# Optimization experiments

Measured on AMD Instinct MI355X. Metric: run time of the kernel, lower is better.

Reference implementation:

```python
import jax, jax.numpy as jnp
import numpy as np

N = 50000
IN_CH = 128
OUT_CH = 64
H1, C1 = 8, 8


def gat_layer(x, src, dst, W, att_src, att_dst, bias, heads, out_ch, concat, n_nodes):
    # x: [N, F_in]; W: [F_in, heads*out_ch]; att_*: [heads, out_ch]; bias: [heads*out_ch] or [out_ch]
    h = (x @ W).reshape(n_nodes, heads, out_ch)              # [N,H,C]
    a_src = jnp.einsum('nhc,hc->nh', h, att_src)             # [N,H]
    a_dst = jnp.einsum('nhc,hc->nh', h, att_dst)             # [N,H]
    e = jax.nn.leaky_relu(a_src[src] + a_dst[dst], 0.2)      # [E,H]
    # segment softmax over incoming edges of each dst node
    m = jax.ops.segment_max(e, dst, num_segments=n_nodes)    # [N,H]
    p = jnp.exp(e - m[dst])                                  # [E,H]
    s = jax.ops.segment_sum(p, dst, num_segments=n_nodes)    # [N,H]
    alpha = p / (s[dst] + 1e-16)                             # [E,H]
    out = jax.ops.segment_sum(h[src] * alpha[:, :, None], dst, num_segments=n_nodes)  # [N,H,C]
    out = out.reshape(n_nodes, heads * out_ch) if concat else out.mean(axis=1)
    return out + bias


def setup_inputs() -> dict:
    key = jax.random.key(0)
    ks = jax.random.split(key, 12)
    E = 1600000
    x = jax.random.normal(ks[0], (N, IN_CH), dtype=jnp.float32)
    edge_index = jax.random.randint(ks[1], (2, E), 0, N, dtype=jnp.int64)
    sc = 0.1
    return {
        'x': x,
        'edge_index': edge_index,
        'W1': jax.random.normal(ks[2], (IN_CH, H1 * C1), dtype=jnp.float32) * sc,
        'att_src1': jax.random.normal(ks[3], (H1, C1), dtype=jnp.float32) * sc,
        'att_dst1': jax.random.normal(ks[4], (H1, C1), dtype=jnp.float32) * sc,
        'b1': jnp.zeros((H1 * C1,), dtype=jnp.float32),
        'W2': jax.random.normal(ks[5], (H1 * C1, OUT_CH), dtype=jnp.float32) * sc,
        'att_src2': jax.random.normal(ks[6], (1, OUT_CH), dtype=jnp.float32) * sc,
        'att_dst2': jax.random.normal(ks[7], (1, OUT_CH), dtype=jnp.float32) * sc,
        'b2': jnp.zeros((OUT_CH,), dtype=jnp.float32),
        'lin_W': jax.random.normal(ks[8], (OUT_CH, 1), dtype=jnp.float32) * sc,
        'lin_b': jnp.zeros((1,), dtype=jnp.float32),
    }


def reference(x, edge_index, W1, att_src1, att_dst1, b1, W2, att_src2, att_dst2, b2, lin_W, lin_b):
    # add self loops (PyG GATConv default)
    loops = jnp.arange(N, dtype=edge_index.dtype)
    src = jnp.concatenate([edge_index[0], loops])
    dst = jnp.concatenate([edge_index[1], loops])
    # dropout layers are identity in eval mode
    h = gat_layer(x, src, dst, W1, att_src1, att_dst1, b1, H1, C1, True, N)
    h = jax.nn.elu(h)
    h = gat_layer(h, src, dst, W2, att_src2, att_dst2, b2, 1, OUT_CH, False, N)
    return h @ lin_W + lin_b
```

## Files before the change

### kernel.cpp

```cpp
#include <hip/hip_runtime.h>
#include <hip/hip_bf16.h>
#include <math.h>

#define NN     50000
#define FIN    128
#define F1     64
#define NH1    8
#define F2     64

#define BSH    256
#define NB     ((NN + BSH - 1) / BSH)
#define BCAP   9472
#define PREB   13
#define MG1B   ((NN + 255) / 256)

typedef __bf16 bf16x8 __attribute__((ext_vector_type(8)));
typedef float  f32x4  __attribute__((ext_vector_type(4)));
typedef unsigned short u16x8 __attribute__((ext_vector_type(8)));


__device__ __forceinline__ float loadF(const void* p, long long i, int fp32) {
    if (fp32) return ((const float*)p)[i];
    return __bfloat162float(((const __hip_bfloat16*)p)[i]);
}
__device__ __forceinline__ int loadI_nt(const void* p, long long i, int i64) {
    if (i64) return (int)__builtin_nontemporal_load(&((const long long*)p)[i]);
    return __builtin_nontemporal_load(&((const int*)p)[i]);
}
__device__ __forceinline__ unsigned short f2bfu(float f) {
    unsigned u = __float_as_uint(f);
    return (unsigned short)((u + 0x7FFFu + ((u >> 16) & 1u)) >> 16);
}
__device__ __forceinline__ float b2f(unsigned short u) {
    return __uint_as_float(((unsigned)u) << 16);
}


__global__ __launch_bounds__(1024) void k_front(
    const void* __restrict__ x, const void* __restrict__ ei, int E, int Etot,
    int* __restrict__ flags,
    const void* __restrict__ W1, const void* __restrict__ W2,
    unsigned short* __restrict__ W1p, unsigned short* __restrict__ W2p,
    int* __restrict__ bcnt, unsigned* __restrict__ binned) {
    __shared__ int s_a, s_b;
    __shared__ int hist[NB], gbase[NB];
    int tid = threadIdx.x;
    if (blockIdx.x < PREB) {
        if (tid == 0) { s_a = 0; s_b = 0; }
        __syncthreads();
        const unsigned short* u = (const unsigned short*)x;
        int cnt = 0;
        for (int i = tid; i < 8192; i += 1024) {
            unsigned short v = u[i];
            if ((v & 0x7F80) == 0x7F80) cnt++;
        }
        if (cnt) atomicAdd(&s_a, cnt);
        const unsigned* e32 = (const unsigned*)ei;
        int nz = 0;
        for (int i = tid; i < 2048; i += 1024) {
            if (e32[2 * i + 1] != 0u) nz++;
        }
        if (nz) atomicAdd(&s_b, nz);
        __syncthreads();
        int fp32 = (s_a > 2) ? 1 : 0;
        if (tid == 0 && blockIdx.x == 0) {
            flags[0] = fp32;
            flags[1] = (s_b == 0) ? 1 : 0;
        }
        int gt = blockIdx.x * 1024 + tid, gs = PREB * 1024;
        for (int i = gt; i < (FIN / 32) * 4 * 512; i += gs) {
            int j = i & 7, l = (i >> 3) & 63, f = i >> 9;
            int kb = f >> 2, nt = f & 3;
            int k = kb * 32 + (l >> 4) * 8 + j, n = nt * 16 + (l & 15);
            W1p[i] = f2bfu(loadF(W1, k * 64 + n, fp32));
        }
        for (int i = gt; i < (F1 / 32) * 4 * 512; i += gs) {
            int j = i & 7, l = (i >> 3) & 63, f = i >> 9;
            int kb = f >> 2, nt = f & 3;
            int k = kb * 32 + (l >> 4) * 8 + j, n = nt * 16 + (l & 15);
            W2p[i] = f2bfu(loadF(W2, k * 64 + n, fp32));
        }
    } else {
        if (tid == 0) s_b = 0;
        for (int i = tid; i < NB; i += 1024) hist[i] = 0;
        __syncthreads();
        const unsigned* e32 = (const unsigned*)ei;
        int nz = 0;
        for (int i = tid; i < 2048; i += 1024) {
            if (e32[2 * i + 1] != 0u) nz++;
        }
        if (nz) atomicAdd(&s_b, nz);
        __syncthreads();
        int i64 = (s_b == 0) ? 1 : 0;
        long long base = (long long)(blockIdx.x - PREB) * 8192;
        unsigned pk[8]; short bb[8];
        #pragma unroll
        for (int u = 0; u < 8; ++u) {
            long long j = base + u * 1024 + tid;
            int s = -1, d = -1;
            if (j < Etot) {
                if (j < E) { s = loadI_nt(ei, j, i64); d = loadI_nt(ei, (long long)E + j, i64); }
                else       { s = d = (int)(j - E); }
            }
            if ((unsigned)s < NN && (unsigned)d < NN) {
                bb[u] = (short)(d >> 8);
                pk[u] = ((unsigned)s << 8) | (unsigned)(d & 255);
                atomicAdd(&hist[bb[u]], 1);
            } else bb[u] = -1;
        }
        __syncthreads();
        for (int i = tid; i < NB; i += 1024) {
            int h = hist[i];
            gbase[i] = h ? atomicAdd(&bcnt[i], h) : 0;
            hist[i] = 0;
        }
        __syncthreads();
        #pragma unroll
        for (int u = 0; u < 8; ++u) {
            if (bb[u] >= 0) {
                int pos = gbase[bb[u]] + atomicAdd(&hist[bb[u]], 1);
                if (pos < BCAP) binned[(size_t)bb[u] * BCAP + pos] = pk[u];
            }
        }
    }
}


__global__ __launch_bounds__(1024) void k_mid(
    const int* __restrict__ bcnt, const unsigned* __restrict__ binned,
    int* __restrict__ offs, int* __restrict__ perm,
    const void* __restrict__ x, const unsigned short* __restrict__ W1p,
    const void* __restrict__ attS, const void* __restrict__ attD,
    __hip_bfloat16* __restrict__ h1, float* __restrict__ a1s,
    float* __restrict__ a1d, const int* __restrict__ flags) {
    __shared__ __align__(16) char smem[33280];
    int tid = threadIdx.x;
    if (blockIdx.x < NB) {
        int* hist = (int*)smem;
        int* cur  = (int*)(smem + 1024);
        int* sd   = (int*)(smem + 2048);
        int bk = blockIdx.x;
        int n0 = bk * BSH;
        if (tid < 256) sd[tid] = (tid < NB) ? min(bcnt[tid], BCAP) : 0;
        __syncthreads();
        for (int off = 1; off < BSH; off <<= 1) {
            int t = 0;
            if (tid < 256 && tid >= off) t = sd[tid - off];
            __syncthreads();
            if (tid < 256) sd[tid] += t;
            __syncthreads();
        }
        int gb = (bk > 0) ? sd[bk - 1] : 0;
        if (bk == 0 && tid == 0) offs[NN] = sd[NB - 1];
        __syncthreads();
        int cnt = bcnt[bk]; if (cnt > BCAP) cnt = BCAP;
        const unsigned* bp = binned + (size_t)bk * BCAP;
        if (tid < 256) hist[tid] = 0;
        __syncthreads();
        for (int i = tid; i < cnt; i += 1024)
            atomicAdd(&hist[bp[i] & 255], 1);
        __syncthreads();
        int myh = (tid < 256) ? hist[tid] : 0;
        if (tid < 256) sd[tid] = myh;
        __syncthreads();
        for (int off = 1; off < BSH; off <<= 1) {
            int t = 0;
            if (tid < 256 && tid >= off) t = sd[tid - off];
            __syncthreads();
            if (tid < 256) sd[tid] += t;
            __syncthreads();
        }
        if (tid < 256) {
            int excl = sd[tid] - myh;
            cur[tid] = gb + excl;
            if (n0 + tid < NN) offs[n0 + tid] = gb + excl;
        }
        __syncthreads();
        for (int i = tid; i < cnt; i += 1024) {
            unsigned pk = bp[i];
            int pos = atomicAdd(&cur[pk & 255], 1);
            perm[pos] = (int)(pk >> 8);
        }
    } else {
        int fp32 = flags[0];
        unsigned short* hl = (unsigned short*)smem;
        float* attSl = (float*)(smem + 32768);
        float* attDl = (float*)(smem + 32768 + 256);
        if (tid < 64) { attSl[tid] = loadF(attS, tid, fp32); attDl[tid] = loadF(attD, tid, fp32); }
        int sub = tid >> 8, t = tid & 255;
        int w = t >> 6, l = t & 63;
        int quad = l >> 4, lm = l & 15;
        int n0 = (blockIdx.x - NB) * 256 + sub * 64;
        unsigned short* hls = hl + sub * 4096;

        bf16x8 bfr[16];
        #pragma unroll
        for (int f = 0; f < 16; ++f)
            bfr[f] = *(const bf16x8*)(W1p + f * 512 + l * 8);

        int nodeA = n0 + w * 16 + lm;
        long long rowA = (nodeA < NN) ? nodeA : 0;
        f32x4 acc[4];
        #pragma unroll
        for (int nt = 0; nt < 4; ++nt) acc[nt] = (f32x4){0.f, 0.f, 0.f, 0.f};

        #pragma unroll
        for (int kb = 0; kb < 4; ++kb) {
            bf16x8 af;
            if (!fp32) {
                af = *(const bf16x8*)((const unsigned short*)x + rowA * FIN + kb * 32 + quad * 8);
            } else {
                const float* xf = (const float*)x + rowA * FIN + kb * 32 + quad * 8;
                union { unsigned short s[8]; bf16x8 v; } tmp;
                #pragma unroll
                for (int j = 0; j < 8; ++j) tmp.s[j] = f2bfu(xf[j]);
                af = tmp.v;
            }
            #pragma unroll
            for (int nt = 0; nt < 4; ++nt)
                acc[nt] = __builtin_amdgcn_mfma_f32_16x16x32_bf16(af, bfr[kb * 4 + nt], acc[nt], 0, 0, 0);
        }

        #pragma unroll
        for (int nt = 0; nt < 4; ++nt) {
            #pragma unroll
            for (int r = 0; r < 4; ++r) {
                int nl = w * 16 + quad * 4 + r;
                int node = n0 + nl;
                int c = nt * 16 + lm;
                unsigned short hb = f2bfu(acc[nt][r]);
                hls[nl * 64 + c] = hb;
                if (node < NN) ((unsigned short*)h1)[(size_t)node * 64 + c] = hb;
            }
        }
        __syncthreads();
        #pragma unroll
        for (int pp = 0; pp < 2; ++pp) {
            int p = t + pp * 256;
            int nl = p >> 3, g = p & 7;
            int node = n0 + nl;
            float ss = 0.f, dd = 0.f;
            #pragma unroll
            for (int j = 0; j < 8; ++j) {
                float hv = b2f(hls[nl * 64 + g * 8 + j]);
                ss += hv * attSl[g * 8 + j];
                dd += hv * attDl[g * 8 + j];
            }
            if (node < NN) {
                a1s[(size_t)node * NH1 + g] = ss;
                a1d[(size_t)node * NH1 + g] = dd;
            }
        }
    }
}


#define HLP 72

__global__ __launch_bounds__(256) void k_agg1f(
    const int* __restrict__ offs, const int* __restrict__ perm,
    const __hip_bfloat16* __restrict__ h1, const float* __restrict__ a1s,
    const float* __restrict__ a1d, const void* __restrict__ b1,
    const unsigned short* __restrict__ W2p,
    const void* __restrict__ attS2, const void* __restrict__ attD2,
    const void* __restrict__ linW,
    float2* __restrict__ g2s, float* __restrict__ a2d,
    int n, const int* __restrict__ flags) {
    int fp32 = flags[0];
    __shared__ __align__(16) unsigned short hl[16 * HLP];
    __shared__ float attSl[64], attDl[64];
    __shared__ float sp[16 * 4], dp[16 * 4], gp[16 * 4];
    int tid = threadIdx.x;
    if (tid < 64) { attSl[tid] = loadF(attS2, tid, fp32); attDl[tid] = loadF(attD2, tid, fp32); }
    int w = tid >> 6, c = tid & 63;
    int n0 = blockIdx.x * 16;
    const unsigned short* hu = (const unsigned short*)h1;

    int g = c >> 3, q = c & 7;
    float b1r[8];
    #pragma unroll
    for (int k = 0; k < 8; ++k) b1r[k] = loadF(b1, q * 8 + k, fp32);

    for (int m = 0; m < 4; ++m) {
        int d = n0 + w * 4 + m;
        if (d < n) {
            int start = offs[d], end = offs[d + 1];
            float adl = a1d[(size_t)d * NH1 + q];
            float accv[8];
            #pragma unroll
            for (int k = 0; k < 8; ++k) accv[k] = 0.f;
            float den = 0.f;
            for (int i = start; i < end; i += 8) {
                int j = i + g;
                int jc = (j < end) ? j : (end - 1);
                int sj = perm[jc];
                float e = a1s[(size_t)sj * NH1 + q] + adl;
                e = fmaxf(e, 0.2f * e);
                float p = (j < end) ? __expf(e) : 0.f;
                den += p;
                u16x8 hv = *(const u16x8*)(hu + (size_t)sj * 64 + q * 8);
                #pragma unroll
                for (int k = 0; k < 8; ++k)
                    accv[k] = fmaf(p, b2f(hv[k]), accv[k]);
            }
            #pragma unroll
            for (int k = 0; k < 8; ++k) {
                accv[k] += __shfl_xor(accv[k], 8, 64);
                accv[k] += __shfl_xor(accv[k], 16, 64);
                accv[k] += __shfl_xor(accv[k], 32, 64);
            }
            den += __shfl_xor(den, 8, 64);
            den += __shfl_xor(den, 16, 64);
            den += __shfl_xor(den, 32, 64);
            float rden = 1.f / (den + 1e-16f);
            if (g == 0) {
                unsigned pk4[4];
                #pragma unroll
                for (int k = 0; k < 4; ++k) {
                    float v0 = fmaf(accv[2 * k],     rden, b1r[2 * k]);
                    float v1 = fmaf(accv[2 * k + 1], rden, b1r[2 * k + 1]);
                    v0 = (v0 > 0.f) ? v0 : expm1f(v0);
                    v1 = (v1 > 0.f) ? v1 : expm1f(v1);
                    pk4[k] = (unsigned)f2bfu(v0) | ((unsigned)f2bfu(v1) << 16);
                }
                *(uint4*)&hl[(w * 4 + m) * HLP + q * 8] =
                    make_uint4(pk4[0], pk4[1], pk4[2], pk4[3]);
            }
        }
    }
    __syncthreads();

    int quad = c >> 4, lm = c & 15;
    bf16x8 bf0 = *(const bf16x8*)(W2p + (0 * 4 + w) * 512 + c * 8);
    bf16x8 bf1 = *(const bf16x8*)(W2p + (1 * 4 + w) * 512 + c * 8);
    bf16x8 af0 = *(const bf16x8*)(hl + lm * HLP + 0 * 32 + quad * 8);
    bf16x8 af1 = *(const bf16x8*)(hl + lm * HLP + 1 * 32 + quad * 8);
    f32x4 acc2 = (f32x4){0.f, 0.f, 0.f, 0.f};
    acc2 = __builtin_amdgcn_mfma_f32_16x16x32_bf16(af0, bf0, acc2, 0, 0, 0);
    acc2 = __builtin_amdgcn_mfma_f32_16x16x32_bf16(af1, bf1, acc2, 0, 0, 0);

    int cg = w * 16 + lm;
    float aSc = attSl[cg], aDc = attDl[cg];
    float lWc = loadF(linW, cg, fp32);
    #pragma unroll
    for (int r = 0; r < 4; ++r) {
        int nl = quad * 4 + r;
        unsigned short hb = f2bfu(acc2[r]);
        float hv = b2f(hb);
        float pvs = hv * aSc, pvd = hv * aDc, pvg = hv * lWc;
        pvs += __shfl_xor(pvs, 1, 64); pvd += __shfl_xor(pvd, 1, 64); pvg += __shfl_xor(pvg, 1, 64);
        pvs += __shfl_xor(pvs, 2, 64); pvd += __shfl_xor(pvd, 2, 64); pvg += __shfl_xor(pvg, 2, 64);
        pvs += __shfl_xor(pvs, 4, 64); pvd += __shfl_xor(pvd, 4, 64); pvg += __shfl_xor(pvg, 4, 64);
        pvs += __shfl_xor(pvs, 8, 64); pvd += __shfl_xor(pvd, 8, 64); pvg += __shfl_xor(pvg, 8, 64);
        if (lm == 0) { sp[nl * 4 + w] = pvs; dp[nl * 4 + w] = pvd; gp[nl * 4 + w] = pvg; }
    }
    __syncthreads();
    if (tid < 16) {
        int node = n0 + tid;
        if (node < n) {
            float ss = sp[tid * 4 + 0] + sp[tid * 4 + 1] + sp[tid * 4 + 2] + sp[tid * 4 + 3];
            float dd = dp[tid * 4 + 0] + dp[tid * 4 + 1] + dp[tid * 4 + 2] + dp[tid * 4 + 3];
            float gg = gp[tid * 4 + 0] + gp[tid * 4 + 1] + gp[tid * 4 + 2] + gp[tid * 4 + 3];
            g2s[node] = make_float2(ss, gg);
            a2d[node] = dd;
        }
    }
}


__global__ __launch_bounds__(256) void k_agg2(
    const int* __restrict__ offs, const int* __restrict__ perm,
    const float2* __restrict__ g2s, const float* __restrict__ a2d,
    const void* __restrict__ b2, const void* __restrict__ linW,
    const void* __restrict__ linb,
    void* __restrict__ out, int n, const int* __restrict__ flags) {
    int fp32 = flags[0];
    int w = threadIdx.x >> 6, c = threadIdx.x & 63;
    int d = blockIdx.x * 4 + w;
    if (d >= n) return;
    int start = offs[d], end = offs[d + 1];
    float ad = a2d[d];
    float acc = 0.f, den = 0.f;
    for (int i = start + c; i < end; i += 64) {
        int s = perm[i];
        float2 ag = g2s[s];
        float e = ag.x + ad;
        e = fmaxf(e, 0.2f * e);
        float p = __expf(e);
        acc = fmaf(p, ag.y, acc);
        den += p;
    }
    float cst = loadF(b2, c, fp32) * loadF(linW, c, fp32);
    #pragma unroll
    for (int off = 1; off < 64; off <<= 1) {
        acc += __shfl_xor(acc, off, 64);
        den += __shfl_xor(den, off, 64);
        cst += __shfl_xor(cst, off, 64);
    }
    if (c == 0) {
        float r = acc / (den + 1e-16f) + cst + loadF(linb, 0, fp32);
        if (fp32) ((float*)out)[d] = r;
        else      ((__hip_bfloat16*)out)[d] = __float2bfloat16(r);
    }
}


static inline char* carve(char*& p, size_t bytes) {
    char* r = p;
    p += (bytes + 255) & ~size_t(255);
    return r;
}

extern "C" void kernel_launch(void* const* d_in, const int* in_sizes, int n_in,
                              void* d_out, int out_size, void* d_ws, size_t ws_size,
                              hipStream_t stream) {
    const void* x     = d_in[0];
    const void* ei    = d_in[1];
    const void* W1    = d_in[2];
    const void* attS1 = d_in[3];
    const void* attD1 = d_in[4];
    const void* b1    = d_in[5];
    const void* W2    = d_in[6];
    const void* attS2 = d_in[7];
    const void* attD2 = d_in[8];
    const void* b2    = d_in[9];
    const void* linW  = d_in[10];
    const void* linb  = d_in[11];

    int E    = in_sizes[1] / 2;
    int Etot = E + NN;

    char* p = (char*)d_ws;
    int*   flags = (int*)carve(p, 256);
    int*   bcnt  = (int*)carve(p, (size_t)NB * 4);
    unsigned short* W1p = (unsigned short*)carve(p, 8192 * 2);
    unsigned short* W2p = (unsigned short*)carve(p, 4096 * 2);
    int*   offs  = (int*)carve(p, (size_t)(NN + 1) * 4);
    int*   perm  = (int*)carve(p, (size_t)Etot * 4);
    unsigned* binned = (unsigned*)carve(p, (size_t)NB * BCAP * 4);
    float*    a1s    = (float*)carve(p, (size_t)NN * NH1 * 4);
    float*    a1d    = (float*)carve(p, (size_t)NN * NH1 * 4);
    __hip_bfloat16* h1 = (__hip_bfloat16*)carve(p, (size_t)NN * F1 * 2);
    float2* g2s = (float2*)carve(p, (size_t)NN * 8);
    float*  a2d = (float*)carve(p, (size_t)NN * 4);

    hipMemsetAsync(bcnt, 0, (size_t)NB * 4, stream);

    int nbin = (Etot + 8191) / 8192;
    k_front<<<PREB + nbin, 1024, 0, stream>>>(x, ei, E, Etot, flags,
                                              W1, W2, W1p, W2p, bcnt, binned);
    k_mid<<<NB + MG1B, 1024, 0, stream>>>(bcnt, binned, offs, perm,
                                          x, W1p, attS1, attD1, h1, a1s, a1d, flags);
    k_agg1f<<<(NN + 15) / 16, 256, 0, stream>>>(offs, perm, h1, a1s, a1d, b1,
                                                W2p, attS2, attD2, linW, g2s, a2d, NN, flags);
    k_agg2<<<(NN + 3) / 4, 256, 0, stream>>>(offs, perm, g2s, a2d, b2, linW, linb, d_out, NN, flags);
}
```

Before: 201.0 us.

## Split layer-1 features into head halves for cache-friendlier gather in aggregation

The layer-1 projected features and source attention logits are split into two half-width arrays (heads 0-3 and 4-7). The aggregation kernel now makes two passes, one per half, each handling 16 edges at a time with 4 lanes per node. Partial sums and denominators go through shared memory before the normalise, ELU and bias epilogue. The intent is to shrink the random-gather working set per pass so it fits better in L2/MALL, at the cost of reading perm and the edge ranges twice. Perm reads also become nontemporal loads.

```diff
diff --git a/kernel.cpp b/kernel.cpp
--- a/kernel.cpp
+++ b/kernel.cpp
@@ -131,7 +131,8 @@
     int* __restrict__ offs, int* __restrict__ perm,
     const void* __restrict__ x, const unsigned short* __restrict__ W1p,
     const void* __restrict__ attS, const void* __restrict__ attD,
-    __hip_bfloat16* __restrict__ h1, float* __restrict__ a1s,
+    __hip_bfloat16* __restrict__ h1lo, __hip_bfloat16* __restrict__ h1hi,
+    float* __restrict__ a1sl, float* __restrict__ a1sh,
     float* __restrict__ a1d, const int* __restrict__ flags) {
     __shared__ __align__(16) char smem[33280];
     int tid = threadIdx.x;
@@ -230,7 +231,10 @@
                 int c = nt * 16 + lm;
                 unsigned short hb = f2bfu(acc[nt][r]);
                 hls[nl * 64 + c] = hb;
-                if (node < NN) ((unsigned short*)h1)[(size_t)node * 64 + c] = hb;
+                if (node < NN) {
+                    if (nt < 2) ((unsigned short*)h1lo)[(size_t)node * 32 + c] = hb;
+                    else        ((unsigned short*)h1hi)[(size_t)node * 32 + (c - 32)] = hb;
+                }
             }
         }
         __syncthreads();
@@ -247,7 +251,8 @@
                 dd += hv * attDl[g * 8 + j];
             }
             if (node < NN) {
-                a1s[(size_t)node * NH1 + g] = ss;
+                if (g < 4) a1sl[(size_t)node * 4 + g] = ss;
+                else       a1sh[(size_t)node * 4 + (g - 4)] = ss;
                 a1d[(size_t)node * NH1 + g] = dd;
             }
         }
@@ -259,7 +264,8 @@
 
 __global__ __launch_bounds__(256) void k_agg1f(
     const int* __restrict__ offs, const int* __restrict__ perm,
-    const __hip_bfloat16* __restrict__ h1, const float* __restrict__ a1s,
+    const __hip_bfloat16* __restrict__ h1lo, const __hip_bfloat16* __restrict__ h1hi,
+    const float* __restrict__ a1sl, const float* __restrict__ a1sh,
     const float* __restrict__ a1d, const void* __restrict__ b1,
     const unsigned short* __restrict__ W2p,
     const void* __restrict__ attS2, const void* __restrict__ attD2,
@@ -268,64 +274,80 @@
     int n, const int* __restrict__ flags) {
     int fp32 = flags[0];
     __shared__ __align__(16) unsigned short hl[16 * HLP];
+    __shared__ __align__(16) float accb[16 * 64];
+    __shared__ float denb[16 * 8];
     __shared__ float attSl[64], attDl[64];
     __shared__ float sp[16 * 4], dp[16 * 4], gp[16 * 4];
     int tid = threadIdx.x;
     if (tid < 64) { attSl[tid] = loadF(attS2, tid, fp32); attDl[tid] = loadF(attD2, tid, fp32); }
     int w = tid >> 6, c = tid & 63;
     int n0 = blockIdx.x * 16;
-    const unsigned short* hu = (const unsigned short*)h1;
-
-    int g = c >> 3, q = c & 7;
-    float b1r[8];
-    #pragma unroll
-    for (int k = 0; k < 8; ++k) b1r[k] = loadF(b1, q * 8 + k, fp32);
-
-    for (int m = 0; m < 4; ++m) {
-        int d = n0 + w * 4 + m;
-        if (d < n) {
-            int start = offs[d], end = offs[d + 1];
-            float adl = a1d[(size_t)d * NH1 + q];
-            float accv[8];
+
+    int g = c >> 2, q = c & 3;
+    for (int half = 0; half < 2; ++half) {
+        const unsigned short* hu = (const unsigned short*)(half ? h1hi : h1lo);
+        const float* as = half ? a1sh : a1sl;
+        for (int m = 0; m < 4; ++m) {
+            int d = n0 + w * 4 + m;
+            if (d < n) {
+                int start = offs[d], end = offs[d + 1];
+                float adl = a1d[(size_t)d * NH1 + half * 4 + q];
+                float accv[8];
+                #pragma unroll
+                for (int k = 0; k < 8; ++k) accv[k] = 0.f;
+                float den = 0.f;
+                for (int i = start; i < end; i += 16) {
+                    int j = i + g;
+                    int jc = (j < end) ? j : (end - 1);
+                    int sj = __builtin_nontemporal_load(&perm[jc]);
+                    float e = as[(size_t)sj * 4 + q] + adl;
+                    e = fmaxf(e, 0.2f * e);
+                    float p = (j < end) ? __expf(e) : 0.f;
+                    den += p;
+                    u16x8 hv = *(const u16x8*)(hu + (size_t)sj * 32 + q * 8);
+                    #pragma unroll
+                    for (int k = 0; k < 8; ++k)
+                        accv[k] = fmaf(p, b2f(hv[k]), accv[k]);
+                }
+                #pragma unroll
+                for (int k = 0; k < 8; ++k) {
+                    accv[k] += __shfl_xor(accv[k], 4, 64);
+                    accv[k] += __shfl_xor(accv[k], 8, 64);
+                    accv[k] += __shfl_xor(accv[k], 16, 64);
+                    accv[k] += __shfl_xor(accv[k], 32, 64);
+                }
+                den += __shfl_xor(den, 4, 64);
+                den += __shfl_xor(den, 8, 64);
+                den += __shfl_xor(den, 16, 64);
+                den += __shfl_xor(den, 32, 64);
+                if (g == 0) {
+                    int nl = w * 4 + m;
+                    *(f32x4*)&accb[nl * 64 + half * 32 + q * 8] =
+                        (f32x4){accv[0], accv[1], accv[2], accv[3]};
+                    *(f32x4*)&accb[nl * 64 + half * 32 + q * 8 + 4] =
+                        (f32x4){accv[4], accv[5], accv[6], accv[7]};
+                    denb[nl * 8 + half * 4 + q] = den;
+                }
+            }
+        }
+    }
+    __syncthreads();
+
+    {
+        int p4 = tid * 4, nl = p4 >> 6, c0 = p4 & 63;
+        int node = n0 + nl;
+        if (node < n) {
+            float rd = 1.f / (denb[nl * 8 + (c0 >> 3)] + 1e-16f);
+            unsigned pk2[2];
             #pragma unroll
-            for (int k = 0; k < 8; ++k) accv[k] = 0.f;
-            float den = 0.f;
-            for (int i = start; i < end; i += 8) {
-                int j = i + g;
-                int jc = (j < end) ? j : (end - 1);
-                int sj = perm[jc];
-                float e = a1s[(size_t)sj * NH1 + q] + adl;
-                e = fmaxf(e, 0.2f * e);
-                float p = (j < end) ? __expf(e) : 0.f;
-                den += p;
-                u16x8 hv = *(const u16x8*)(hu + (size_t)sj * 64 + q * 8);
-                #pragma unroll
-                for (int k = 0; k < 8; ++k)
-                    accv[k] = fmaf(p, b2f(hv[k]), accv[k]);
-            }
-            #pragma unroll
-            for (int k = 0; k < 8; ++k) {
-                accv[k] += __shfl_xor(accv[k], 8, 64);
-                accv[k] += __shfl_xor(accv[k], 16, 64);
-                accv[k] += __shfl_xor(accv[k], 32, 64);
-            }
-            den += __shfl_xor(den, 8, 64);
-            den += __shfl_xor(den, 16, 64);
-            den += __shfl_xor(den, 32, 64);
-            float rden = 1.f / (den + 1e-16f);
-            if (g == 0) {
-                unsigned pk4[4];
-                #pragma unroll
-                for (int k = 0; k < 4; ++k) {
-                    float v0 = fmaf(accv[2 * k],     rden, b1r[2 * k]);
-                    float v1 = fmaf(accv[2 * k + 1], rden, b1r[2 * k + 1]);
-                    v0 = (v0 > 0.f) ? v0 : expm1f(v0);
-                    v1 = (v1 > 0.f) ? v1 : expm1f(v1);
-                    pk4[k] = (unsigned)f2bfu(v0) | ((unsigned)f2bfu(v1) << 16);
-                }
-                *(uint4*)&hl[(w * 4 + m) * HLP + q * 8] =
-                    make_uint4(pk4[0], pk4[1], pk4[2], pk4[3]);
-            }
+            for (int k2 = 0; k2 < 2; ++k2) {
+                float v0 = fmaf(accb[nl * 64 + c0 + 2 * k2],     rd, loadF(b1, c0 + 2 * k2, fp32));
+                float v1 = fmaf(accb[nl * 64 + c0 + 2 * k2 + 1], rd, loadF(b1, c0 + 2 * k2 + 1, fp32));
+                v0 = (v0 > 0.f) ? v0 : expm1f(v0);
+                v1 = (v1 > 0.f) ? v1 : expm1f(v1);
+                pk2[k2] = (unsigned)f2bfu(v0) | ((unsigned)f2bfu(v1) << 16);
+            }
+            *(uint2*)&hl[nl * HLP + c0] = make_uint2(pk2[0], pk2[1]);
         }
     }
     __syncthreads();
@@ -438,9 +460,11 @@
     int*   offs  = (int*)carve(p, (size_t)(NN + 1) * 4);
     int*   perm  = (int*)carve(p, (size_t)Etot * 4);
     unsigned* binned = (unsigned*)carve(p, (size_t)NB * BCAP * 4);
-    float*    a1s    = (float*)carve(p, (size_t)NN * NH1 * 4);
+    float*    a1sl   = (float*)carve(p, (size_t)NN * 4 * 4);
+    float*    a1sh   = (float*)carve(p, (size_t)NN * 4 * 4);
     float*    a1d    = (float*)carve(p, (size_t)NN * NH1 * 4);
-    __hip_bfloat16* h1 = (__hip_bfloat16*)carve(p, (size_t)NN * F1 * 2);
+    __hip_bfloat16* h1lo = (__hip_bfloat16*)carve(p, (size_t)NN * 32 * 2);
+    __hip_bfloat16* h1hi = (__hip_bfloat16*)carve(p, (size_t)NN * 32 * 2);
     float2* g2s = (float2*)carve(p, (size_t)NN * 8);
     float*  a2d = (float*)carve(p, (size_t)NN * 4);
 
@@ -450,8 +474,10 @@
     k_front<<<PREB + nbin, 1024, 0, stream>>>(x, ei, E, Etot, flags,
                                               W1, W2, W1p, W2p, bcnt, binned);
     k_mid<<<NB + MG1B, 1024, 0, stream>>>(bcnt, binned, offs, perm,
-                                          x, W1p, attS1, attD1, h1, a1s, a1d, flags);
-    k_agg1f<<<(NN + 15) / 16, 256, 0, stream>>>(offs, perm, h1, a1s, a1d, b1,
-                                                W2p, attS2, attD2, linW, g2s, a2d, NN, flags);
+                                          x, W1p, attS1, attD1, h1lo, h1hi,
+                                          a1sl, a1sh, a1d, flags);
+    k_agg1f<<<(NN + 15) / 16, 256, 0, stream>>>(offs, perm, h1lo, h1hi, a1sl, a1sh,
+                                                a1d, b1, W2p, attS2, attD2, linW,
+                                                g2s, a2d, NN, flags);
     k_agg2<<<(NN + 3) / 4, 256, 0, stream>>>(offs, perm, g2s, a2d, b2, linW, linb, d_out, NN, flags);
 }
```

Measured after the change: 227.1 us. 13.0% more time.
